# Kernel optimization log

Measured on AMD Instinct MI355X. Metric: run time of the kernel, lower is better.

Reference implementation:

```python
import jax, jax.numpy as jnp
import numpy as np

B, T, H = 256, 1024, 512  # batch, max_len, hidden_dim
PAD = -1.0


def setup_inputs() -> dict:
    key = jax.random.key(0)
    ks = jax.random.split(key, 8)
    # ragged lengths in [1, T], suffix padding with -1 (pack_padded_sequence semantics)
    lengths = jax.random.randint(ks[0], (B,), 1, T + 1)
    vals = jax.random.uniform(ks[1], (B, T), minval=0.0, maxval=10.0)
    t = jnp.arange(T)[None, :]
    trajectories = jnp.where(t < lengths[:, None], vals, PAD)
    k = 1.0 / np.sqrt(H)  # torch default uniform init bound
    u = lambda kk, shape: jax.random.uniform(kk, shape, minval=-k, maxval=k, dtype=jnp.float32)
    return dict(
        trajectories=trajectories,
        W_ih=u(ks[2], (4 * H, 1)),   # LSTM input weights (input_dim = 1)
        W_hh=u(ks[3], (4 * H, H)),   # LSTM recurrent weights
        b_ih=u(ks[4], (4 * H,)),
        b_hh=u(ks[5], (4 * H,)),
        fc_W=u(ks[6], (T, H)),       # per-sample fc uses first L rows
        fc_b=u(ks[7], (T,)),
    )


def _lstm_last(trajectories, W_ih, W_hh, b_ih, b_hh):
    """Batched LSTM over ragged sequences; returns hidden state at step L-1 per sample."""
    valid = trajectories != PAD          # [B,T] bool, suffix padding
    x = trajectories[..., None]          # [B,T,1]
    b = b_ih + b_hh                      # [4H]

    def step(carry, inp):
        h, c = carry
        x_t, m_t = inp                   # x_t [B,1], m_t [B]
        gates = x_t @ W_ih.T + h @ W_hh.T + b   # [B,4H], torch gate order i,f,g,o
        i, f, g, o = jnp.split(gates, 4, axis=-1)
        i = jax.nn.sigmoid(i)
        f = jax.nn.sigmoid(f)
        g = jnp.tanh(g)
        o = jax.nn.sigmoid(o)
        c_new = f * c + i * g
        h_new = o * jnp.tanh(c_new)
        m = m_t[:, None]                 # freeze state past each sample's length
        return (jnp.where(m, h_new, h), jnp.where(m, c_new, c)), None

    init = (jnp.zeros((B, H), trajectories.dtype), jnp.zeros((B, H), trajectories.dtype))
    (h, _), _ = jax.lax.scan(step, init, (jnp.swapaxes(x, 0, 1), valid.T))
    return h, valid


def reference(trajectories, W_ih, W_hh, b_ih, b_hh, fc_W, fc_b):
    h, valid = _lstm_last(trajectories, W_ih, W_hh, b_ih, b_hh)  # h: [B,H]
    lengths = valid.sum(axis=1)                                   # [B]
    logits = h @ fc_W.T + fc_b                                    # [B,T]
    pos = jnp.arange(T)[None, :] < lengths[:, None]               # first L positions per sample
    neg = jnp.finfo(logits.dtype).min
    probs = jax.nn.softmax(jnp.where(pos, logits, neg), axis=-1)  # softmax over first L logits
    return jnp.where(pos, probs, jnp.asarray(1.0, logits.dtype))  # F.pad(..., value=1)
```

## Files before the change

### kernel.cpp

```cpp
#include <hip/hip_runtime.h>

#define TT 1024
#define BB 256
#define HH 512
#define G4 2048
#define NG 32
#define SG 8
#define NJ 16
#define RW 128
#define JW 32
#define FS 32

typedef _Float16 half2v __attribute__((ext_vector_type(2)));
typedef _Float16 half8  __attribute__((ext_vector_type(8)));
typedef __fp16   fp16x2 __attribute__((ext_vector_type(2)));
typedef float    f32x4  __attribute__((ext_vector_type(4)));
typedef unsigned int uint;

union U32H  { uint u; half2v h; fp16x2 g; };
union U128H { uint4 u; half8 h; };
union U64F  { unsigned long long u; float f[2]; };

__global__ __launch_bounds__(256) void prep_k(
    const float* __restrict__ Whh, const float* __restrict__ fcW,
    const float* __restrict__ bih, const float* __restrict__ bhh,
    uint* __restrict__ Wpk16, float* __restrict__ fcWT, float* __restrict__ bsum,
    float* __restrict__ hbuf, int* __restrict__ flags)
{
    int n  = blockDim.x * gridDim.x;
    int i0 = blockIdx.x * blockDim.x + threadIdx.x;
    for (int i = i0; i < NJ * 8 * 16 * 64 * 4; i += n) {
        int d  = i & 3;
        int l  = (i >> 2) & 63;
        int kk = (i >> 8) & 15;
        int w  = (i >> 12) & 7;
        int jg = (i >> 15) & 15;
        int rl   = w * 16 + (l & 15);
        int gate = rl >> 5, jj = rl & 31;
        int grow = gate * HH + jg * JW + jj;
        int k    = kk * 32 + ((l >> 4) & 3) * 8 + 2 * d;
        half2v p;
        p.x = (_Float16)Whh[grow * HH + k];
        p.y = (_Float16)Whh[grow * HH + k + 1];
        U32H x; x.h = p;
        Wpk16[i] = x.u;
    }
    for (int i = i0; i < HH * TT; i += n) {
        int k = i >> 10, t = i & (TT - 1);
        fcWT[i] = fcW[t * HH + k];
    }
    for (int i = i0; i < G4; i += n) bsum[i] = bih[i] + bhh[i];
    for (int i = i0; i < 2 * BB * HH; i += n) hbuf[i] = 0.f;
    for (int i = i0; i < NG * NJ * FS; i += n) flags[i] = 0;
}

__global__ __launch_bounds__(256) void lens_k(const float* __restrict__ traj,
                                              int* __restrict__ len)
{
    int b = blockIdx.x;
    int cnt = 0;
    for (int i = threadIdx.x; i < TT; i += 256)
        cnt += (traj[b * TT + i] != -1.0f) ? 1 : 0;
    for (int o = 32; o > 0; o >>= 1) cnt += __shfl_down(cnt, o, 64);
    __shared__ int s4[4];
    if ((threadIdx.x & 63) == 0) s4[threadIdx.x >> 6] = cnt;
    __syncthreads();
    if (threadIdx.x == 0) len[b] = s4[0] + s4[1] + s4[2] + s4[3];
}

__global__ __launch_bounds__(256) void sort_k(const int* __restrict__ len,
                                              int* __restrict__ perm,
                                              int* __restrict__ glen)
{
    __shared__ int L[256];
    __shared__ int P[256];
    int tid = threadIdx.x;
    L[tid] = len[tid];
    __syncthreads();
    int l = L[tid], r = 0;
    for (int b = 0; b < 256; ++b) {
        int lb = L[b];
        r += (lb > l) || (lb == l && b < tid);
    }
    P[r] = tid;
    __syncthreads();
    perm[tid] = P[tid];
    if (tid < NG) glen[tid] = L[P[tid * SG]];
}

__device__ __forceinline__ void wait_flags(const int* __restrict__ flg, int target, int tid)
{
    int lane = tid & 63;
    while (true) {
        int v = target;
        if (lane < NJ)
            v = __hip_atomic_load(&flg[lane * FS], __ATOMIC_RELAXED, __HIP_MEMORY_SCOPE_AGENT);
        if (__all(v >= target)) break;
        __builtin_amdgcn_s_sleep(1);
    }
}

__device__ __forceinline__ void issue_pf(const float* __restrict__ hbuf, int g, int T,
                                         float (&pf)[8], int tid)
{
    const float* hsrc = hbuf + ((size_t)(T & 1) * BB + g * SG) * HH;
    int s = tid >> 6, l = tid & 63;
    const unsigned long long* p = (const unsigned long long*)(hsrc + (size_t)s * HH);
    #pragma unroll
    for (int q = 0; q < 4; ++q) {
        U64F v;
        v.u = __hip_atomic_load(&p[q * 64 + l], __ATOMIC_RELAXED, __HIP_MEMORY_SCOPE_AGENT);
        pf[2 * q]     = v.f[0];
        pf[2 * q + 1] = v.f[1];
    }
}

__device__ __forceinline__ void do_phase(
    int g, int t, int tid, int jg,
    const float* __restrict__ traj, const int* __restrict__ osL,
    uint* __restrict__ hsL, float* __restrict__ carryL, float* __restrict__ gbL,
    float* __restrict__ xsL, float* __restrict__ mkL,
    const float* __restrict__ wih_s, const float* __restrict__ bsum_s,
    const half8 (&wf)[16], float& creg,
    float (&pfCur)[8], float (&pfN)[8], int pfGrp, int pfT, int pfMode,
    float* __restrict__ hbuf, int* __restrict__ flags)
{
    const int w  = tid >> 6;
    const int l  = tid & 63;
    const int sm = l & 15;
    const int ks = (l >> 4) & 3;

    {
        int s = w;
        int swz = (s & 7) << 2;
        #pragma unroll
        for (int q = 0; q < 4; ++q) {
            U32H x;
            x.g = __builtin_amdgcn_cvt_pkrtz(pfCur[2 * q], pfCur[2 * q + 1]);
            int k2 = q * 64 + l;
            hsL[s * 256 + (k2 ^ swz)] = x.u;
            if (q == (jg >> 2) && (l >> 4) == (jg & 3)) {
                carryL[s * 32 + 2 * (l & 15)]     = pfCur[2 * q];
                carryL[s * 32 + 2 * (l & 15) + 1] = pfCur[2 * q + 1];
            }
        }
    }
    if (tid < SG) {
        float v = traj[(size_t)osL[tid] * TT + t];
        xsL[tid] = v;
        mkL[tid] = (v != -1.0f) ? 1.f : 0.f;
    }
    __syncthreads();

    f32x4 acc0 = {0.f, 0.f, 0.f, 0.f}, acc1 = {0.f, 0.f, 0.f, 0.f};
    {
        const int smswz = (sm & 7) << 2;
        const int bbase = sm * 256;
        #pragma unroll
        for (int kk = 0; kk < 16; kk += 2) {
            U128H b0, b1;
            b0.u = *(const uint4*)&hsL[bbase + ((kk * 16 + ks * 4) ^ smswz)];
            b1.u = *(const uint4*)&hsL[bbase + (((kk + 1) * 16 + ks * 4) ^ smswz)];
            acc0 = __builtin_amdgcn_mfma_f32_16x16x32_f16(wf[kk],     b0.h, acc0, 0, 0, 0);
            acc1 = __builtin_amdgcn_mfma_f32_16x16x32_f16(wf[kk + 1], b1.h, acc1, 0, 0, 0);
        }
    }

    if (sm < SG) {
        float xv = xsL[sm];
        #pragma unroll
        for (int r = 0; r < 4; ++r) {
            int rl = w * 16 + ks * 4 + r;
            float pre = fmaf(xv, wih_s[rl], (acc0[r] + acc1[r]) + bsum_s[rl]);
            bool isg = ((rl >> 5) == 2);
            float sc = isg ? 2.f : 1.f;
            float sg = 1.f / (1.f + __expf(-pre * sc));
            gbL[sm * 136 + rl] = fmaf(sg, sc, isg ? -1.f : 0.f);
        }
    }

    if (pfMode == 1) {
        wait_flags(flags + pfGrp * NJ * FS, pfT, tid);
        issue_pf(hbuf, pfGrp, pfT, pfN, tid);
    }
    __syncthreads();

    if (tid < 256) {
        int s = tid >> 5, jj = tid & 31;
        float hv;
        if (mkL[s] > 0.f) {
            float iv = gbL[s * 136 + jj];
            float fv = gbL[s * 136 + 32 + jj];
            float gv = gbL[s * 136 + 64 + jj];
            float ov = gbL[s * 136 + 96 + jj];
            float cn = fmaf(fv, creg, iv * gv);
            creg = cn;
            float e = __expf(2.f * cn);
            hv = ov * (1.f - 2.f / (e + 1.f));
        } else {
            hv = carryL[s * 32 + jj];
        }
        float* hout = hbuf + ((size_t)((t + 1) & 1) * BB + g * SG) * HH;
        __hip_atomic_store(&hout[s * HH + jg * JW + jj], hv, __ATOMIC_RELAXED,
                           __HIP_MEMORY_SCOPE_AGENT);
    }
    __syncthreads();
    if (tid == 0)
        __hip_atomic_store(&flags[g * NJ * FS + jg * FS], t + 1, __ATOMIC_RELAXED,
                           __HIP_MEMORY_SCOPE_AGENT);
    if (pfMode == 2) {
        wait_flags(flags + pfGrp * NJ * FS, pfT, tid);
        issue_pf(hbuf, pfGrp, pfT, pfN, tid);
    }
}

__global__ __launch_bounds__(512, 2) void lstm_persist(
    const float* __restrict__ traj, const float* __restrict__ Wih,
    const uint* __restrict__ Wpk16, const float* __restrict__ bsum,
    float* __restrict__ hbuf,
    const int* __restrict__ perm, const int* __restrict__ glen,
    int* __restrict__ flags)
{
    __shared__ __align__(16) float smem[23040];
    __shared__ float xsm[2][SG], mkm[2][SG];
    __shared__ int   osm[2][SG];
    __shared__ float wih_s[RW], bsum_s[RW];

    uint*  const hsA16  = (uint*)smem;
    uint*  const hsB16  = (uint*)(smem + 4096);
    float* const carryA = smem + 8192;
    float* const carryB = smem + 8448;
    float* const gbA    = smem + 8704;
    float* const gbB    = smem + 9792;

    const int wg  = blockIdx.x;
    const int p   = wg & 15;
    const int jg  = wg >> 4;
    const int tid = threadIdx.x;
    const int gA = p, gB = 31 - p;

    if (tid < 2 * SG) {
        int gi = tid >> 3, s = tid & 7;
        osm[gi][s] = perm[((gi == 0) ? gA : gB) * SG + s];
    }
    if (tid < RW) {
        int gate = tid >> 5, jj = tid & 31;
        int grow = gate * HH + jg * JW + jj;
        wih_s[tid]  = Wih[grow];
        bsum_s[tid] = bsum[grow];
    }
    const int glenA = glen[gA], glenB = glen[gB];

    half8 wf[16];
    {
        const int w = tid >> 6, l = tid & 63;
        const uint4* wp = (const uint4*)Wpk16;
        const int base = (jg * 8 + w) * 1024 + l;
        #pragma unroll
        for (int kk = 0; kk < 16; ++kk) {
            U128H u; u.u = wp[base + kk * 64];
            wf[kk] = u.h;
        }
    }

    float cA = 0.f, cB = 0.f;
    float pfA[8], pfB[8];
    #pragma unroll
    for (int q = 0; q < 8; ++q) { pfA[q] = 0.f; pfB[q] = 0.f; }
    __syncthreads();

    for (int t = 0; t < glenA; ++t) {
        if (t < glenB) {
            do_phase(gA, t, tid, jg, traj, osm[0], hsA16, carryA, gbA, xsm[0], mkm[0],
                     wih_s, bsum_s, wf, cA, pfA, pfB, gB, t, 1, hbuf, flags);
            do_phase(gB, t, tid, jg, traj, osm[1], hsB16, carryB, gbB, xsm[1], mkm[1],
                     wih_s, bsum_s, wf, cB, pfB, pfA, gA, t + 1, 1, hbuf, flags);
        } else {
            do_phase(gA, t, tid, jg, traj, osm[0], hsA16, carryA, gbA, xsm[0], mkm[0],
                     wih_s, bsum_s, wf, cA, pfA, pfA, gA, t + 1,
                     (t + 1 < glenA) ? 2 : 0, hbuf, flags);
        }
    }
}

__global__ __launch_bounds__(256) void epi_k(
    const float* __restrict__ hbuf, const float* __restrict__ fcWT,
    const float* __restrict__ fcb, const int* __restrict__ len,
    const int* __restrict__ perm, const int* __restrict__ glen,
    float* __restrict__ out)
{
    __shared__ float hb[HH];
    __shared__ float lg[TT];
    __shared__ float red[4];
    const int slot = blockIdx.x, tid = threadIdx.x;
    const int ob = perm[slot];
    const int par = glen[slot >> 3] & 1;

    const float* hfin = hbuf + ((size_t)par * BB + slot) * HH;
    for (int i = tid; i < HH; i += 256) hb[i] = hfin[i];
    __syncthreads();

    const int t0 = tid * 4;
    float a0 = fcb[t0], a1 = fcb[t0 + 1], a2 = fcb[t0 + 2], a3 = fcb[t0 + 3];
    #pragma unroll 8
    for (int k = 0; k < HH; ++k) {
        float4 w = *(const float4*)&fcWT[k * TT + t0];
        float hv = hb[k];
        a0 += w.x * hv; a1 += w.y * hv; a2 += w.z * hv; a3 += w.w * hv;
    }
    lg[t0] = a0; lg[t0 + 1] = a1; lg[t0 + 2] = a2; lg[t0 + 3] = a3;
    __syncthreads();

    const int L = len[ob];
    float mx = -3.4e38f;
    for (int i = tid; i < L; i += 256) mx = fmaxf(mx, lg[i]);
    for (int o = 32; o > 0; o >>= 1) mx = fmaxf(mx, __shfl_down(mx, o, 64));
    if ((tid & 63) == 0) red[tid >> 6] = mx;
    __syncthreads();
    mx = fmaxf(fmaxf(red[0], red[1]), fmaxf(red[2], red[3]));
    __syncthreads();

    float sm = 0.f;
    for (int i = tid; i < L; i += 256) {
        float e = __expf(lg[i] - mx);
        lg[i] = e;
        sm += e;
    }
    for (int o = 32; o > 0; o >>= 1) sm += __shfl_down(sm, o, 64);
    if ((tid & 63) == 0) red[tid >> 6] = sm;
    __syncthreads();
    sm = red[0] + red[1] + red[2] + red[3];
    float inv = 1.f / sm;

    for (int i = tid; i < TT; i += 256)
        out[ob * TT + i] = (i < L) ? lg[i] * inv : 1.0f;
}

extern "C" void kernel_launch(void* const* d_in, const int* in_sizes, int n_in,
                              void* d_out, int out_size, void* d_ws, size_t ws_size,
                              hipStream_t stream)
{
    const float* traj = (const float*)d_in[0];
    const float* Wih  = (const float*)d_in[1];
    const float* Whh  = (const float*)d_in[2];
    const float* bih  = (const float*)d_in[3];
    const float* bhh  = (const float*)d_in[4];
    const float* fcW  = (const float*)d_in[5];
    const float* fcb  = (const float*)d_in[6];
    float* out = (float*)d_out;

    uint*  Wpk16 = (uint*)d_ws;
    float* fcWT  = (float*)(Wpk16 + NJ * 8 * 16 * 64 * 4);
    float* bsum  = fcWT + HH * TT;
    float* hbuf  = bsum + G4;
    int*   len   = (int*)(hbuf + 2 * BB * HH);
    int*   perm  = len + BB;
    int*   glen  = perm + BB;
    int*   flags = glen + NG;

    prep_k<<<2048, 256, 0, stream>>>(Whh, fcW, bih, bhh, Wpk16, fcWT, bsum, hbuf, flags);
    lens_k<<<BB, 256, 0, stream>>>(traj, len);
    sort_k<<<1, 256, 0, stream>>>(len, perm, glen);

    {
        const float* traj_l = traj; const float* wih_l = Wih;
        const uint* wpk_l = Wpk16;  const float* bsum_l = bsum;
        float* hbuf_l = hbuf;
        const int* perm_l = perm;   const int* glen_l = glen;
        int* flags_l = flags;
        void* args[] = { (void*)&traj_l, (void*)&wih_l, (void*)&wpk_l, (void*)&bsum_l,
                         (void*)&hbuf_l, (void*)&perm_l, (void*)&glen_l, (void*)&flags_l };
        (void)hipLaunchCooperativeKernel((const void*)lstm_persist, dim3(256), dim3(512),
                                         args, 0, stream);
    }

    epi_k<<<BB, 256, 0, stream>>>(hbuf, fcWT, fcb, len, perm, glen, out);
}
```

Baseline: 2.494 ms.

## Fuse paired sample groups into one 16-column MFMA phase with in-register gate math

```diff
diff --git a/kernel.cpp b/kernel.cpp
--- a/kernel.cpp
+++ b/kernel.cpp
@@ -16,10 +16,11 @@
 typedef __fp16   fp16x2 __attribute__((ext_vector_type(2)));
 typedef float    f32x4  __attribute__((ext_vector_type(4)));
 typedef unsigned int uint;
+typedef unsigned long long u64t;
 
 union U32H  { uint u; half2v h; fp16x2 g; };
 union U128H { uint4 u; half8 h; };
-union U64F  { unsigned long long u; float f[2]; };
+union U64F  { u64t u; float f[2]; };
 
 __global__ __launch_bounds__(256) void prep_k(
     const float* __restrict__ Whh, const float* __restrict__ fcW,
@@ -35,9 +36,9 @@
         int kk = (i >> 8) & 15;
         int w  = (i >> 12) & 7;
         int jg = (i >> 15) & 15;
-        int rl   = w * 16 + (l & 15);
-        int gate = rl >> 5, jj = rl & 31;
-        int grow = gate * HH + jg * JW + jj;
+        int m    = l & 15;
+        int gate = m & 3, jjq = m >> 2;
+        int grow = gate * HH + jg * JW + w * 4 + jjq;
         int k    = kk * 32 + ((l >> 4) & 3) * 8 + 2 * d;
         half2v p;
         p.x = (_Float16)Whh[grow * HH + k];
@@ -100,120 +101,6 @@
     }
 }
 
-__device__ __forceinline__ void issue_pf(const float* __restrict__ hbuf, int g, int T,
-                                         float (&pf)[8], int tid)
-{
-    const float* hsrc = hbuf + ((size_t)(T & 1) * BB + g * SG) * HH;
-    int s = tid >> 6, l = tid & 63;
-    const unsigned long long* p = (const unsigned long long*)(hsrc + (size_t)s * HH);
-    #pragma unroll
-    for (int q = 0; q < 4; ++q) {
-        U64F v;
-        v.u = __hip_atomic_load(&p[q * 64 + l], __ATOMIC_RELAXED, __HIP_MEMORY_SCOPE_AGENT);
-        pf[2 * q]     = v.f[0];
-        pf[2 * q + 1] = v.f[1];
-    }
-}
-
-__device__ __forceinline__ void do_phase(
-    int g, int t, int tid, int jg,
-    const float* __restrict__ traj, const int* __restrict__ osL,
-    uint* __restrict__ hsL, float* __restrict__ carryL, float* __restrict__ gbL,
-    float* __restrict__ xsL, float* __restrict__ mkL,
-    const float* __restrict__ wih_s, const float* __restrict__ bsum_s,
-    const half8 (&wf)[16], float& creg,
-    float (&pfCur)[8], float (&pfN)[8], int pfGrp, int pfT, int pfMode,
-    float* __restrict__ hbuf, int* __restrict__ flags)
-{
-    const int w  = tid >> 6;
-    const int l  = tid & 63;
-    const int sm = l & 15;
-    const int ks = (l >> 4) & 3;
-
-    {
-        int s = w;
-        int swz = (s & 7) << 2;
-        #pragma unroll
-        for (int q = 0; q < 4; ++q) {
-            U32H x;
-            x.g = __builtin_amdgcn_cvt_pkrtz(pfCur[2 * q], pfCur[2 * q + 1]);
-            int k2 = q * 64 + l;
-            hsL[s * 256 + (k2 ^ swz)] = x.u;
-            if (q == (jg >> 2) && (l >> 4) == (jg & 3)) {
-                carryL[s * 32 + 2 * (l & 15)]     = pfCur[2 * q];
-                carryL[s * 32 + 2 * (l & 15) + 1] = pfCur[2 * q + 1];
-            }
-        }
-    }
-    if (tid < SG) {
-        float v = traj[(size_t)osL[tid] * TT + t];
-        xsL[tid] = v;
-        mkL[tid] = (v != -1.0f) ? 1.f : 0.f;
-    }
-    __syncthreads();
-
-    f32x4 acc0 = {0.f, 0.f, 0.f, 0.f}, acc1 = {0.f, 0.f, 0.f, 0.f};
-    {
-        const int smswz = (sm & 7) << 2;
-        const int bbase = sm * 256;
-        #pragma unroll
-        for (int kk = 0; kk < 16; kk += 2) {
-            U128H b0, b1;
-            b0.u = *(const uint4*)&hsL[bbase + ((kk * 16 + ks * 4) ^ smswz)];
-            b1.u = *(const uint4*)&hsL[bbase + (((kk + 1) * 16 + ks * 4) ^ smswz)];
-            acc0 = __builtin_amdgcn_mfma_f32_16x16x32_f16(wf[kk],     b0.h, acc0, 0, 0, 0);
-            acc1 = __builtin_amdgcn_mfma_f32_16x16x32_f16(wf[kk + 1], b1.h, acc1, 0, 0, 0);
-        }
-    }
-
-    if (sm < SG) {
-        float xv = xsL[sm];
-        #pragma unroll
-        for (int r = 0; r < 4; ++r) {
-            int rl = w * 16 + ks * 4 + r;
-            float pre = fmaf(xv, wih_s[rl], (acc0[r] + acc1[r]) + bsum_s[rl]);
-            bool isg = ((rl >> 5) == 2);
-            float sc = isg ? 2.f : 1.f;
-            float sg = 1.f / (1.f + __expf(-pre * sc));
-            gbL[sm * 136 + rl] = fmaf(sg, sc, isg ? -1.f : 0.f);
-        }
-    }
-
-    if (pfMode == 1) {
-        wait_flags(flags + pfGrp * NJ * FS, pfT, tid);
-        issue_pf(hbuf, pfGrp, pfT, pfN, tid);
-    }
-    __syncthreads();
-
-    if (tid < 256) {
-        int s = tid >> 5, jj = tid & 31;
-        float hv;
-        if (mkL[s] > 0.f) {
-            float iv = gbL[s * 136 + jj];
-            float fv = gbL[s * 136 + 32 + jj];
-            float gv = gbL[s * 136 + 64 + jj];
-            float ov = gbL[s * 136 + 96 + jj];
-            float cn = fmaf(fv, creg, iv * gv);
-            creg = cn;
-            float e = __expf(2.f * cn);
-            hv = ov * (1.f - 2.f / (e + 1.f));
-        } else {
-            hv = carryL[s * 32 + jj];
-        }
-        float* hout = hbuf + ((size_t)((t + 1) & 1) * BB + g * SG) * HH;
-        __hip_atomic_store(&hout[s * HH + jg * JW + jj], hv, __ATOMIC_RELAXED,
-                           __HIP_MEMORY_SCOPE_AGENT);
-    }
-    __syncthreads();
-    if (tid == 0)
-        __hip_atomic_store(&flags[g * NJ * FS + jg * FS], t + 1, __ATOMIC_RELAXED,
-                           __HIP_MEMORY_SCOPE_AGENT);
-    if (pfMode == 2) {
-        wait_flags(flags + pfGrp * NJ * FS, pfT, tid);
-        issue_pf(hbuf, pfGrp, pfT, pfN, tid);
-    }
-}
-
 __global__ __launch_bounds__(512, 2) void lstm_persist(
     const float* __restrict__ traj, const float* __restrict__ Wih,
     const uint* __restrict__ Wpk16, const float* __restrict__ bsum,
@@ -222,34 +109,27 @@
     int* __restrict__ flags)
 {
     __shared__ __align__(16) float smem[23040];
-    __shared__ float xsm[2][SG], mkm[2][SG];
-    __shared__ int   osm[2][SG];
+    __shared__ float xsm[16], mkm[16];
+    __shared__ int   osm[16];
     __shared__ float wih_s[RW], bsum_s[RW];
 
-    uint*  const hsA16  = (uint*)smem;
-    uint*  const hsB16  = (uint*)(smem + 4096);
-    float* const carryA = smem + 8192;
-    float* const carryB = smem + 8448;
-    float* const gbA    = smem + 8704;
-    float* const gbB    = smem + 9792;
-
-    const int wg  = blockIdx.x;
-    const int p   = wg & 15;
-    const int jg  = wg >> 4;
-    const int tid = threadIdx.x;
-    const int gA = p, gB = 31 - p;
-
-    if (tid < 2 * SG) {
-        int gi = tid >> 3, s = tid & 7;
-        osm[gi][s] = perm[((gi == 0) ? gA : gB) * SG + s];
-    }
+    uint* const hs16 = (uint*)smem;
+
+    const int wg   = blockIdx.x;
+    const int slot = wg & 15;
+    const int jg   = wg >> 4;
+    const int tid  = threadIdx.x;
+    const int gA = slot, gB = 31 - slot;
+
+    if (tid < 16)
+        osm[tid] = perm[(tid < 8) ? (gA * SG + tid) : (gB * SG + tid - 8)];
     if (tid < RW) {
-        int gate = tid >> 5, jj = tid & 31;
-        int grow = gate * HH + jg * JW + jj;
+        int m = tid & 15;
+        int grow = (m & 3) * HH + jg * JW + (tid >> 4) * 4 + (m >> 2);
         wih_s[tid]  = Wih[grow];
         bsum_s[tid] = bsum[grow];
     }
-    const int glenA = glen[gA], glenB = glen[gB];
+    const int glenA = glen[gA];
 
     half8 wf[16];
     {
@@ -263,22 +143,101 @@
         }
     }
 
-    float cA = 0.f, cB = 0.f;
-    float pfA[8], pfB[8];
+    const int w  = tid >> 6;
+    const int l  = tid & 63;
+    const int sm = l & 15;
+    const int ks = (l >> 4) & 3;
+    const int jj = w * 4 + ks;
+    const int sslot = (sm < 8) ? (gA * SG + sm) : (gB * SG + sm - 8);
+
+    float creg = 0.f, hreg = 0.f;
+    float pf[16];
     #pragma unroll
-    for (int q = 0; q < 8; ++q) { pfA[q] = 0.f; pfB[q] = 0.f; }
+    for (int q = 0; q < 16; ++q) pf[q] = 0.f;
+
+    int* const flg = flags + slot * NJ * FS;
     __syncthreads();
 
     for (int t = 0; t < glenA; ++t) {
-        if (t < glenB) {
-            do_phase(gA, t, tid, jg, traj, osm[0], hsA16, carryA, gbA, xsm[0], mkm[0],
-                     wih_s, bsum_s, wf, cA, pfA, pfB, gB, t, 1, hbuf, flags);
-            do_phase(gB, t, tid, jg, traj, osm[1], hsB16, carryB, gbB, xsm[1], mkm[1],
-                     wih_s, bsum_s, wf, cB, pfB, pfA, gA, t + 1, 1, hbuf, flags);
-        } else {
-            do_phase(gA, t, tid, jg, traj, osm[0], hsA16, carryA, gbA, xsm[0], mkm[0],
-                     wih_s, bsum_s, wf, cA, pfA, pfA, gA, t + 1,
-                     (t + 1 < glenA) ? 2 : 0, hbuf, flags);
+        {
+            int s = tid >> 6;
+            int swz = (s & 7) << 2;
+            #pragma unroll
+            for (int q = 0; q < 4; ++q) {
+                int k2 = q * 64 + l;
+                U32H a, b;
+                a.g = __builtin_amdgcn_cvt_pkrtz(pf[2 * q], pf[2 * q + 1]);
+                b.g = __builtin_amdgcn_cvt_pkrtz(pf[8 + 2 * q], pf[9 + 2 * q]);
+                hs16[s * 256 + (k2 ^ swz)]       = a.u;
+                hs16[(s + 8) * 256 + (k2 ^ swz)] = b.u;
+            }
+        }
+        if (tid < 16) {
+            float v = traj[(size_t)osm[tid] * TT + t];
+            xsm[tid] = v;
+            mkm[tid] = (v != -1.0f) ? 1.f : 0.f;
+        }
+        __syncthreads();
+
+        f32x4 acc0 = {0.f, 0.f, 0.f, 0.f}, acc1 = {0.f, 0.f, 0.f, 0.f};
+        {
+            const int smswz = (sm & 7) << 2;
+            const int bbase = sm * 256;
+            #pragma unroll
+            for (int kk = 0; kk < 16; kk += 2) {
+                U128H b0, b1;
+                b0.u = *(const uint4*)&hs16[bbase + ((kk * 16 + ks * 4) ^ smswz)];
+                b1.u = *(const uint4*)&hs16[bbase + (((kk + 1) * 16 + ks * 4) ^ smswz)];
+                acc0 = __builtin_amdgcn_mfma_f32_16x16x32_f16(wf[kk],     b0.h, acc0, 0, 0, 0);
+                acc1 = __builtin_amdgcn_mfma_f32_16x16x32_f16(wf[kk + 1], b1.h, acc1, 0, 0, 0);
+            }
+        }
+
+        {
+            float xv = xsm[sm];
+            float rb = (float)(w * 16 + ks * 4);
+            int   r0 = w * 16 + ks * 4;
+            float p0 = fmaf(xv, wih_s[r0 + 0], (acc0[0] + acc1[0]) + bsum_s[r0 + 0]);
+            float p1 = fmaf(xv, wih_s[r0 + 1], (acc0[1] + acc1[1]) + bsum_s[r0 + 1]);
+            float p2 = fmaf(xv, wih_s[r0 + 2], (acc0[2] + acc1[2]) + bsum_s[r0 + 2]);
+            float p3 = fmaf(xv, wih_s[r0 + 3], (acc0[3] + acc1[3]) + bsum_s[r0 + 3]);
+            (void)rb;
+            float iv = 1.f / (1.f + __expf(-p0));
+            float fv = 1.f / (1.f + __expf(-p1));
+            float gv = 1.f - 2.f / (__expf(2.f * p2) + 1.f);
+            float ov = 1.f / (1.f + __expf(-p3));
+            float cn = fmaf(fv, creg, iv * gv);
+            float hn = ov * (1.f - 2.f / (__expf(2.f * cn) + 1.f));
+            bool  mk = mkm[sm] > 0.f;
+            creg = mk ? cn : creg;
+            hreg = mk ? hn : hreg;
+            float* hout = hbuf + (size_t)((t + 1) & 1) * BB * HH;
+            __hip_atomic_store(&hout[(size_t)sslot * HH + jg * JW + jj], hreg,
+                               __ATOMIC_RELAXED, __HIP_MEMORY_SCOPE_AGENT);
+        }
+        __syncthreads();
+
+        if (tid == 0)
+            __hip_atomic_store(&flg[jg * FS], t + 1, __ATOMIC_RELAXED,
+                               __HIP_MEMORY_SCOPE_AGENT);
+
+        if (t + 1 < glenA) {
+            wait_flags(flg, t + 1, tid);
+            const float* hin = hbuf + (size_t)((t + 1) & 1) * BB * HH;
+            const u64t* pA = (const u64t*)(hin + (size_t)(gA * SG + (tid >> 6)) * HH);
+            const u64t* pB = (const u64t*)(hin + (size_t)(gB * SG + (tid >> 6)) * HH);
+            #pragma unroll
+            for (int q = 0; q < 4; ++q) {
+                U64F va, vb;
+                va.u = __hip_atomic_load(&pA[q * 64 + l], __ATOMIC_RELAXED,
+                                         __HIP_MEMORY_SCOPE_AGENT);
+                vb.u = __hip_atomic_load(&pB[q * 64 + l], __ATOMIC_RELAXED,
+                                         __HIP_MEMORY_SCOPE_AGENT);
+                pf[2 * q]     = va.f[0];
+                pf[2 * q + 1] = va.f[1];
+                pf[8 + 2 * q] = vb.f[0];
+                pf[9 + 2 * q] = vb.f[1];
+            }
         }
     }
 }
@@ -294,7 +253,9 @@
     __shared__ float red[4];
     const int slot = blockIdx.x, tid = threadIdx.x;
     const int ob = perm[slot];
-    const int par = glen[slot >> 3] & 1;
+    const int g = slot >> 3;
+    const int lead = (g < 16) ? g : (31 - g);
+    const int par = glen[lead] & 1;
 
     const float* hfin = hbuf + ((size_t)par * BB + slot) * HH;
     for (int i = tid; i < HH; i += 256) hb[i] = hfin[i];
```

Result: slower. 3.091 ms (+23.9%).
